# Kernel tuning notes

Measured on AMD Instinct MI355X. Metric: run time of the kernel, lower is better.

Reference implementation:

```python
import jax, jax.numpy as jnp
import numpy as np

N_QUBITS = 8   # out_channels = number of wires
KERNEL = 4     # kernel_size
N_LAYERS = 4
STRIDE = 1
PAD = 1


def _rx(t):
    c = jnp.cos(t * 0.5).astype(jnp.complex64)
    s = jnp.sin(t * 0.5).astype(jnp.complex64)
    return jnp.stack([jnp.stack([c, -1j * s]), jnp.stack([-1j * s, c])])


def _ry(t):
    c = jnp.cos(t * 0.5).astype(jnp.complex64)
    s = jnp.sin(t * 0.5).astype(jnp.complex64)
    return jnp.stack([jnp.stack([c, -s]), jnp.stack([s, c])])


def _rz(t):
    e = jnp.exp(-0.5j * t.astype(jnp.complex64))
    z = jnp.zeros((), jnp.complex64)
    return jnp.stack([jnp.stack([e, z]), jnp.stack([z, jnp.conj(e)])])


def _ap1(state, U, w):
    # apply 2x2 gate U on qubit axis w of state shaped (2,)*N_QUBITS
    s = jnp.moveaxis(state, w, -1)
    s = s @ U.T
    return jnp.moveaxis(s, -1, w)


def _cnot(state, c, t):
    s0 = jax.lax.index_in_dim(state, 0, axis=c, keepdims=True)
    s1 = jax.lax.index_in_dim(state, 1, axis=c, keepdims=True)
    return jnp.concatenate([s0, jnp.flip(s1, axis=t)], axis=c)


def _ansatz(state, wl):  # wl: (N_QUBITS, 3) angles for layer i (custom_layers)
    for j in range(N_QUBITS):
        c, t = (j, j + 1) if j < N_QUBITS - 1 else (0, j)
        state = _ap1(state, _rx(wl[j, 0]), j)
        state = _cnot(state, c, t)
        state = _ap1(state, _ry(wl[j, 1]), j)
        state = _cnot(state, c, t)
        state = _ap1(state, _rz(wl[j, 2]), j)
    return state


def _circuit(inputs, weights):
    # inputs: (KERNEL,) patch; weights: (N_LAYERS+1, N_QUBITS, 3)
    state = jnp.zeros((2,) * N_QUBITS, jnp.complex64).at[(0,) * N_QUBITS].set(1.0)
    state = _ansatz(state, weights[0])
    for i in range(1, N_LAYERS + 1):
        w = 0
        for _ in range(N_QUBITS // KERNEL):  # 'parallel': re-upload data each layer
            for k in range(KERNEL):
                state = _ap1(state, _ry(inputs[k]), w + k)
            w += KERNEL
        state = _ansatz(state, weights[i])
    probs = state.real ** 2 + state.imag ** 2
    sign = jnp.array([1.0, -1.0], jnp.float32)
    z = [jnp.sum(probs, axis=tuple(a for a in range(N_QUBITS) if a != j)) @ sign
         for j in range(N_QUBITS)]
    return jnp.stack(z)  # (N_QUBITS,) <PauliZ_j>


def _forward(vector, weights):
    bs, ch, l = vector.shape
    if ch > 1:
        vector = vector.mean(axis=-2).reshape(bs, 1, l)
    v = jnp.pad(vector, ((0, 0), (0, 0), (PAD, PAD)))
    l_out = (l + 2 * PAD - KERNEL) // STRIDE + 1
    idx = jnp.arange(l_out)[:, None] * STRIDE + jnp.arange(KERNEL)  # (l_out, K)
    patches = v[:, 0, :][:, idx].reshape(bs * l_out, KERNEL)
    q = jax.vmap(_circuit, in_axes=(0, None))(patches, weights)  # (bs*l_out, N_QUBITS)
    out = q.reshape(bs, l_out, N_QUBITS).transpose(0, 2, 1)  # (bs, C, l_out)
    out = jax.nn.relu(out)
    return jnp.max(out, axis=-1, keepdims=True)  # (bs, C, 1)


def setup_inputs() -> dict:
    key = jax.random.key(0)
    k1, k2 = jax.random.split(key)
    vector = jax.random.normal(k1, (8, 1, 512), jnp.float32)
    # flax nn.initializers.normal() default stddev = 0.01
    weights = jax.random.normal(k2, (N_LAYERS + 1, N_QUBITS, 3), jnp.float32) * 0.01
    return {"vector": vector, "weights": weights}


def reference(vector, weights):
    return _forward(vector, weights)
```

## Files before the change

kernel.cpp:

```cpp
#include <hip/hip_runtime.h>

#define NQ 8
#define KK 4
#define LIN 512
#define LOUT 511
#define BATCH 8
#define NCIRC (BATCH * LOUT)

__device__ float g_tab[240];
__device__ float g_st0[512];

template<int M> __device__ __forceinline__ float lx(float v) {
    if constexpr (M == 1)
        return __builtin_bit_cast(float, __builtin_amdgcn_update_dpp(
            0, __builtin_bit_cast(int, v), 0xB1, 0xF, 0xF, true));
    else if constexpr (M == 2)
        return __builtin_bit_cast(float, __builtin_amdgcn_update_dpp(
            0, __builtin_bit_cast(int, v), 0x4E, 0xF, 0xF, true));
    else if constexpr (M == 3)
        return __builtin_bit_cast(float, __builtin_amdgcn_update_dpp(
            0, __builtin_bit_cast(int, v), 0x1B, 0xF, 0xF, true));
    else if constexpr (M < 32)
        return __builtin_bit_cast(float, __builtin_amdgcn_ds_swizzle(
            __builtin_bit_cast(int, v), (M << 10) | 0x1F));
    else
        return __shfl_xor(v, M, 64);
}

template<int BP>
__device__ __forceinline__ void g_rx4(float (&sr)[4], float (&si)[4], float c, float s, int lane) {
    if constexpr (BP >= 2) {
        constexpr int M = 1 << (BP - 2);
        #pragma unroll
        for (int r = 0; r < 4; ++r) {
            float orr = lx<M>(sr[r]), oii = lx<M>(si[r]);
            float nr = c * sr[r] + s * oii;
            float ni = c * si[r] - s * orr;
            sr[r] = nr; si[r] = ni;
        }
    } else if constexpr (BP == 1) {
        #pragma unroll
        for (int p = 0; p < 2; ++p) {
            const int a = p, b = p + 2;
            float ar = sr[a], ai = si[a], br = sr[b], bi = si[b];
            sr[a] = c*ar + s*bi;  si[a] = c*ai - s*br;
            sr[b] = c*br + s*ai;  si[b] = c*bi - s*ar;
        }
    } else {
        #pragma unroll
        for (int p = 0; p < 2; ++p) {
            const int a = 2*p, b = 2*p + 1;
            float ar = sr[a], ai = si[a], br = sr[b], bi = si[b];
            sr[a] = c*ar + s*bi;  si[a] = c*ai - s*br;
            sr[b] = c*br + s*ai;  si[b] = c*bi - s*ar;
        }
    }
}

template<int BP>
__device__ __forceinline__ void g_rz4(float (&sr)[4], float (&si)[4], float c, float s, int lane) {
    if constexpr (BP >= 2) {
        const float t = ((lane >> (BP - 2)) & 1) ? -s : s;
        #pragma unroll
        for (int r = 0; r < 4; ++r) {
            float nr = c * sr[r] + t * si[r];
            float ni = c * si[r] - t * sr[r];
            sr[r] = nr; si[r] = ni;
        }
    } else if constexpr (BP == 1) {
        #pragma unroll
        for (int r = 0; r < 4; ++r) {
            const float t = (r < 2) ? s : -s;
            float nr = c * sr[r] + t * si[r];
            float ni = c * si[r] - t * sr[r];
            sr[r] = nr; si[r] = ni;
        }
    } else {
        #pragma unroll
        for (int r = 0; r < 4; ++r) {
            const float t = ((r & 1) == 0) ? s : -s;
            float nr = c * sr[r] + t * si[r];
            float ni = c * si[r] - t * sr[r];
            sr[r] = nr; si[r] = ni;
        }
    }
}

template<int BPC, int BPT>
__device__ __forceinline__ void g_fry4(float (&sr)[4], float (&si)[4], float c, float s, int lane) {
    if constexpr (BPT >= 2) {
        constexpr int M = (1 << (BPC - 2)) | (1 << (BPT - 2));
        const float sg = ((lane >> (BPC - 2)) & 1) ? s : -s;
        #pragma unroll
        for (int r = 0; r < 4; ++r) {
            float orr = lx<M>(sr[r]), oii = lx<M>(si[r]);
            sr[r] = c * sr[r] + sg * orr;
            si[r] = c * si[r] + sg * oii;
        }
    } else if constexpr (BPT == 1) {
        constexpr int M = 1 << (BPC - 2);
        const float sg = ((lane >> (BPC - 2)) & 1) ? s : -s;
        float pr[4], pi[4];
        #pragma unroll
        for (int r = 0; r < 4; ++r) { pr[r] = lx<M>(sr[r ^ 2]); pi[r] = lx<M>(si[r ^ 2]); }
        #pragma unroll
        for (int r = 0; r < 4; ++r) { sr[r] = c*sr[r] + sg*pr[r]; si[r] = c*si[r] + sg*pi[r]; }
    } else if constexpr (BPC == 1) {
        float t0r = sr[0], t0i = si[0], t1r = sr[1], t1i = si[1];
        sr[0] = c*sr[0] - s*sr[3];  si[0] = c*si[0] - s*si[3];
        sr[1] = c*sr[1] - s*sr[2];  si[1] = c*si[1] - s*si[2];
        sr[2] = c*sr[2] + s*t1r;    si[2] = c*si[2] + s*t1i;
        sr[3] = c*sr[3] + s*t0r;    si[3] = c*si[3] + s*t0i;
    } else {
        constexpr int M = 1 << (BPC - 2);
        const float sg = ((lane >> (BPC - 2)) & 1) ? s : -s;
        float pr[4], pi[4];
        #pragma unroll
        for (int r = 0; r < 4; ++r) { pr[r] = lx<M>(sr[r ^ 1]); pi[r] = lx<M>(si[r ^ 1]); }
        #pragma unroll
        for (int r = 0; r < 4; ++r) { sr[r] = c*sr[r] + sg*pr[r]; si[r] = c*si[r] + sg*pi[r]; }
    }
}

template<int J>
__device__ __forceinline__ void astep4(float (&sr)[4], float (&si)[4],
                                       const float* __restrict__ t48, int lane) {
    constexpr int CQ = (J < 7) ? J : 0;
    constexpr int TQ = (J < 7) ? (J + 1) : 7;
    constexpr int BP = 7 - J, BPC = 7 - CQ, BPT = 7 - TQ;
    g_rx4<BP>(sr, si, t48[J*6 + 0], t48[J*6 + 1], lane);
    g_fry4<BPC, BPT>(sr, si, t48[J*6 + 2], t48[J*6 + 3], lane);
    g_rz4<BP>(sr, si, t48[J*6 + 4], t48[J*6 + 5], lane);
}

template<int LB>
__device__ __forceinline__ void rx_lane(float (&sr)[16], float (&si)[16], float c, float s) {
    constexpr int M = 1 << LB;
    #pragma unroll
    for (int r = 0; r < 16; ++r) {
        float orr = lx<M>(sr[r]), oii = lx<M>(si[r]);
        float nr = c * sr[r] + s * oii;
        float ni = c * si[r] - s * orr;
        sr[r] = nr; si[r] = ni;
    }
}

template<int LB>
__device__ __forceinline__ void ry_lane(float (&sr)[16], float (&si)[16], float c, float s, int pos) {
    constexpr int M = 1 << LB;
    const float sg = ((pos >> LB) & 1) ? s : -s;
    #pragma unroll
    for (int r = 0; r < 16; ++r) {
        float orr = lx<M>(sr[r]), oii = lx<M>(si[r]);
        sr[r] = c * sr[r] + sg * orr;
        si[r] = c * si[r] + sg * oii;
    }
}

template<int LB>
__device__ __forceinline__ void rz_lane(float (&sr)[16], float (&si)[16], float c, float s, int pos) {
    const float t = ((pos >> LB) & 1) ? -s : s;
    #pragma unroll
    for (int r = 0; r < 16; ++r) {
        float nr = c * sr[r] + t * si[r];
        float ni = c * si[r] - t * sr[r];
        sr[r] = nr; si[r] = ni;
    }
}

template<int RB>
__device__ __forceinline__ void rx_reg(float (&sr)[16], float (&si)[16], float c, float s) {
    constexpr int m = 1 << RB;
    #pragma unroll
    for (int r = 0; r < 16; ++r) {
        if ((r & m) == 0) {
            const int a = r, b = r | m;
            float ar = sr[a], ai = si[a], br = sr[b], bi = si[b];
            sr[a] = c*ar + s*bi;  si[a] = c*ai - s*br;
            sr[b] = c*br + s*ai;  si[b] = c*bi - s*ar;
        }
    }
}

template<int RB>
__device__ __forceinline__ void ry_reg(float (&sr)[16], float (&si)[16], float c, float s) {
    constexpr int m = 1 << RB;
    #pragma unroll
    for (int r = 0; r < 16; ++r) {
        if ((r & m) == 0) {
            const int a = r, b = r | m;
            float ar = sr[a], ai = si[a], br = sr[b], bi = si[b];
            sr[a] = c*ar - s*br;  si[a] = c*ai - s*bi;
            sr[b] = s*ar + c*br;  si[b] = s*ai + c*bi;
        }
    }
}

template<int RB>
__device__ __forceinline__ void rz_reg(float (&sr)[16], float (&si)[16], float c, float s) {
    #pragma unroll
    for (int r = 0; r < 16; ++r) {
        const float t = ((r >> RB) & 1) ? -s : s;
        float nr = c * sr[r] + t * si[r];
        float ni = c * si[r] - t * sr[r];
        sr[r] = nr; si[r] = ni;
    }
}

template<int LBc, int LBt>
__device__ __forceinline__ void fry_ll(float (&sr)[16], float (&si)[16], float c, float s, int pos) {
    constexpr int M = (1 << LBc) | (1 << LBt);
    const float sg = ((pos >> LBc) & 1) ? s : -s;
    #pragma unroll
    for (int r = 0; r < 16; ++r) {
        float orr = lx<M>(sr[r]), oii = lx<M>(si[r]);
        sr[r] = c * sr[r] + sg * orr;
        si[r] = c * si[r] + sg * oii;
    }
}

template<int LBc, int RBt>
__device__ __forceinline__ void fry_lr(float (&sr)[16], float (&si)[16], float c, float s, int pos) {
    constexpr int M = 1 << LBc;
    constexpr int mt = 1 << RBt;
    const float sg = ((pos >> LBc) & 1) ? s : -s;
    float pr[16], pi[16];
    #pragma unroll
    for (int r = 0; r < 16; ++r) { pr[r] = lx<M>(sr[r ^ mt]); pi[r] = lx<M>(si[r ^ mt]); }
    #pragma unroll
    for (int r = 0; r < 16; ++r) { sr[r] = c*sr[r] + sg*pr[r]; si[r] = c*si[r] + sg*pi[r]; }
}

template<int RBc, int RBt>
__device__ __forceinline__ void fry_rr(float (&sr)[16], float (&si)[16], float c, float s) {
    constexpr int mm = (1 << RBc) | (1 << RBt);
    float nr[16], ni[16];
    #pragma unroll
    for (int r = 0; r < 16; ++r) {
        const float sg = ((r >> RBc) & 1) ? s : -s;
        nr[r] = c*sr[r] + sg*sr[r ^ mm];
        ni[r] = c*si[r] + sg*si[r ^ mm];
    }
    #pragma unroll
    for (int r = 0; r < 16; ++r) { sr[r] = nr[r]; si[r] = ni[r]; }
}

__device__ __forceinline__ void ansatz16(float (&sr)[16], float (&si)[16],
                                         const float* __restrict__ t, int pos) {
    rx_lane<3>(sr, si, t[0], t[1]);   fry_ll<3,2>(sr, si, t[2], t[3], pos);   rz_lane<3>(sr, si, t[4], t[5], pos);
    rx_lane<2>(sr, si, t[6], t[7]);   fry_ll<2,1>(sr, si, t[8], t[9], pos);   rz_lane<2>(sr, si, t[10], t[11], pos);
    rx_lane<1>(sr, si, t[12], t[13]); fry_ll<1,0>(sr, si, t[14], t[15], pos); rz_lane<1>(sr, si, t[16], t[17], pos);
    rx_lane<0>(sr, si, t[18], t[19]); fry_lr<0,3>(sr, si, t[20], t[21], pos); rz_lane<0>(sr, si, t[22], t[23], pos);
    rx_reg<3>(sr, si, t[24], t[25]);  fry_rr<3,2>(sr, si, t[26], t[27]);      rz_reg<3>(sr, si, t[28], t[29]);
    rx_reg<2>(sr, si, t[30], t[31]);  fry_rr<2,1>(sr, si, t[32], t[33]);      rz_reg<2>(sr, si, t[34], t[35]);
    rx_reg<1>(sr, si, t[36], t[37]);  fry_rr<1,0>(sr, si, t[38], t[39]);      rz_reg<1>(sr, si, t[40], t[41]);
    rx_reg<0>(sr, si, t[42], t[43]);  fry_lr<3,0>(sr, si, t[44], t[45], pos); rz_reg<0>(sr, si, t[46], t[47]);
}

__device__ __forceinline__ void reup16(float (&sr)[16], float (&si)[16],
                                       const float (&xc)[4], const float (&xs)[4], int pos) {
    ry_lane<3>(sr, si, xc[0], xs[0], pos);  ry_reg<3>(sr, si, xc[0], xs[0]);
    ry_lane<2>(sr, si, xc[1], xs[1], pos);  ry_reg<2>(sr, si, xc[1], xs[1]);
    ry_lane<1>(sr, si, xc[2], xs[2], pos);  ry_reg<1>(sr, si, xc[2], xs[2]);
    ry_lane<0>(sr, si, xc[3], xs[3], pos);  ry_reg<0>(sr, si, xc[3], xs[3]);
}

template<int ST>
__device__ __forceinline__ void bstage16(float (&z)[8], int pos) {
    constexpr int M = 1 << ST;
    #pragma unroll
    for (int q = 0; q < 8; ++q) {
        float o = lx<M>(z[q]);
        if (q < 4 && (3 - q) == ST)
            z[q] = ((pos >> ST) & 1) ? (o - z[q]) : (z[q] - o);
        else
            z[q] += o;
    }
}

__global__ __launch_bounds__(256) void prep_kernel(const float* __restrict__ wts,
                                                   float* __restrict__ out) {
    __shared__ float tt[240];
    const int t = threadIdx.x;
    if (t < 120) {
        float a = 0.5f * wts[t];
        float cv = __cosf(a), sv = __sinf(a);
        g_tab[2*t] = cv;  g_tab[2*t + 1] = sv;
        tt[2*t] = cv;     tt[2*t + 1] = sv;
    }
    if (t >= 192 && t < 192 + BATCH * NQ) out[t - 192] = 0.0f;
    __syncthreads();
    if (t < 64) {
        const int lane = t;
        float sr[4] = {0.f, 0.f, 0.f, 0.f};
        float si[4] = {0.f, 0.f, 0.f, 0.f};
        if (lane == 0) sr[0] = 1.0f;
        astep4<0>(sr, si, tt, lane); astep4<1>(sr, si, tt, lane);
        astep4<2>(sr, si, tt, lane); astep4<3>(sr, si, tt, lane);
        astep4<4>(sr, si, tt, lane); astep4<5>(sr, si, tt, lane);
        astep4<6>(sr, si, tt, lane); astep4<7>(sr, si, tt, lane);
        #pragma unroll
        for (int r = 0; r < 4; ++r) {
            g_st0[(lane*4 + r)*2]     = sr[r];
            g_st0[(lane*4 + r)*2 + 1] = si[r];
        }
    }
}

__global__ __launch_bounds__(256, 1) void quanv_kernel(const float* __restrict__ vec,
                                                       float* __restrict__ out) {
    const int tid = threadIdx.x;
    const int pos = tid & 15;
    int circ = blockIdx.x * 16 + (tid >> 4);
    if (circ > NCIRC - 1) circ = NCIRC - 1;
    const int b = circ / LOUT;
    const int op = circ - b * LOUT;

    float xc[4], xs[4];
    #pragma unroll
    for (int k = 0; k < KK; ++k) {
        int idx = op - 1 + k;
        int ic = idx < 0 ? 0 : (idx > LIN - 1 ? LIN - 1 : idx);
        float xv = vec[b * LIN + ic];
        xv = (idx == ic) ? xv : 0.0f;
        float a = 0.5f * xv;
        xs[k] = __sinf(a); xc[k] = __cosf(a);
    }

    float sr[16], si[16];
    {
        const float4* st4 = (const float4*)g_st0;
        #pragma unroll
        for (int h = 0; h < 8; ++h) {
            float4 v4 = st4[pos * 8 + h];
            sr[2*h]   = v4.x; si[2*h]   = v4.y;
            sr[2*h+1] = v4.z; si[2*h+1] = v4.w;
        }
    }

    #pragma unroll 1
    for (int L = 1; L <= 4; ++L) {
        reup16(sr, si, xc, xs, pos);
        ansatz16(sr, si, g_tab + L * 48, pos);
    }

    float p[16];
    #pragma unroll
    for (int r = 0; r < 16; ++r) p[r] = sr[r]*sr[r] + si[r]*si[r];
    float pl = 0.f, z4 = 0.f, z5 = 0.f, z6 = 0.f, z7 = 0.f;
    #pragma unroll
    for (int r = 0; r < 16; ++r) {
        pl += p[r];
        z4 += ((r >> 3) & 1) ? -p[r] : p[r];
        z5 += ((r >> 2) & 1) ? -p[r] : p[r];
        z6 += ((r >> 1) & 1) ? -p[r] : p[r];
        z7 += ( r       & 1) ? -p[r] : p[r];
    }
    float z[8];
    z[0] = pl; z[1] = pl; z[2] = pl; z[3] = pl;
    z[4] = z4; z[5] = z5; z[6] = z6; z[7] = z7;

    bstage16<0>(z, pos); bstage16<1>(z, pos); bstage16<2>(z, pos); bstage16<3>(z, pos);

    __shared__ float zsh[16][NQ];
    __shared__ int bsh[16];
    const int g = tid >> 4;
    if (pos == 0) {
        bsh[g] = b;
        #pragma unroll
        for (int q = 0; q < NQ; ++q) zsh[g][q] = fmaxf(z[q], 0.0f);
    }
    __syncthreads();
    if (tid < 128) {
        const int gg = tid >> 3, q = tid & 7;
        const bool leader = (gg == 0) || (bsh[gg] != bsh[gg - 1]);
        if (leader) {
            float m = zsh[gg][q];
            for (int g2 = gg + 1; g2 < 16 && bsh[g2] == bsh[gg]; ++g2)
                m = fmaxf(m, zsh[g2][q]);
            atomicMax((unsigned int*)(out + bsh[gg] * NQ + q), __float_as_uint(m));
        }
    }
}

extern "C" void kernel_launch(void* const* d_in, const int* in_sizes, int n_in,
                              void* d_out, int out_size, void* d_ws, size_t ws_size,
                              hipStream_t stream) {
    const float* vec = (const float*)d_in[0];
    const float* wts = (const float*)d_in[1];
    float* out = (float*)d_out;

    hipLaunchKernelGGL(prep_kernel, dim3(1), dim3(256), 0, stream, wts, out);
    const int blocks = (NCIRC + 15) / 16;
    hipLaunchKernelGGL(quanv_kernel, dim3(blocks), dim3(256), 0, stream, vec, out);
}
```

Before: 79.95 us.

## Split each circuit's statevector across 32 lanes with 8 amplitudes per thread

Each simulated circuit now uses 32 threads holding 8 complex amplitudes each instead of 16 threads holding 16, so one more qubit is mapped onto lanes and handled with cross-lane DPP/swizzle exchanges. This halves the per-thread register state and drops the launch-bounds occupancy limit of 1, which should allow more waves per CU. The last layer's RZ gates are skipped because they only change phases and do not affect the Z expectations, and the final CNOT-RY-CNOT is rewritten as a controlled-sign RY. The trade-off is more cross-lane shuffles per gate, a different reduction tree, and twice as many blocks.

```diff
diff --git a/kernel.cpp b/kernel.cpp
--- a/kernel.cpp
+++ b/kernel.cpp
@@ -20,6 +20,9 @@
     else if constexpr (M == 3)
         return __builtin_bit_cast(float, __builtin_amdgcn_update_dpp(
             0, __builtin_bit_cast(int, v), 0x1B, 0xF, 0xF, true));
+    else if constexpr (M == 8)
+        return __builtin_bit_cast(float, __builtin_amdgcn_update_dpp(
+            0, __builtin_bit_cast(int, v), 0x128, 0xF, 0xF, true));
     else if constexpr (M < 32)
         return __builtin_bit_cast(float, __builtin_amdgcn_ds_swizzle(
             __builtin_bit_cast(int, v), (M << 10) | 0x1F));
@@ -122,22 +125,35 @@
     }
 }
 
+__device__ __forceinline__ void g_cry4_q7(float (&sr)[4], float (&si)[4], float c, float s, int lane) {
+    const float se = ((lane >> 5) & 1) ? -s : s;
+    #pragma unroll
+    for (int p = 0; p < 2; ++p) {
+        const int a = 2*p, b = 2*p + 1;
+        float ar = sr[a], ai = si[a], br = sr[b], bi = si[b];
+        sr[a] = c*ar - se*br;  si[a] = c*ai - se*bi;
+        sr[b] = se*ar + c*br;  si[b] = se*ai + c*bi;
+    }
+}
+
 template<int J>
 __device__ __forceinline__ void astep4(float (&sr)[4], float (&si)[4],
                                        const float* __restrict__ t48, int lane) {
-    constexpr int CQ = (J < 7) ? J : 0;
-    constexpr int TQ = (J < 7) ? (J + 1) : 7;
-    constexpr int BP = 7 - J, BPC = 7 - CQ, BPT = 7 - TQ;
+    constexpr int BP = 7 - J;
     g_rx4<BP>(sr, si, t48[J*6 + 0], t48[J*6 + 1], lane);
-    g_fry4<BPC, BPT>(sr, si, t48[J*6 + 2], t48[J*6 + 3], lane);
+    if constexpr (J < 7) {
+        g_fry4<7 - J, 6 - J>(sr, si, t48[J*6 + 2], t48[J*6 + 3], lane);
+    } else {
+        g_cry4_q7(sr, si, t48[J*6 + 2], t48[J*6 + 3], lane);
+    }
     g_rz4<BP>(sr, si, t48[J*6 + 4], t48[J*6 + 5], lane);
 }
 
 template<int LB>
-__device__ __forceinline__ void rx_lane(float (&sr)[16], float (&si)[16], float c, float s) {
+__device__ __forceinline__ void rx_lane(float (&sr)[8], float (&si)[8], float c, float s) {
     constexpr int M = 1 << LB;
     #pragma unroll
-    for (int r = 0; r < 16; ++r) {
+    for (int r = 0; r < 8; ++r) {
         float orr = lx<M>(sr[r]), oii = lx<M>(si[r]);
         float nr = c * sr[r] + s * oii;
         float ni = c * si[r] - s * orr;
@@ -146,11 +162,11 @@
 }
 
 template<int LB>
-__device__ __forceinline__ void ry_lane(float (&sr)[16], float (&si)[16], float c, float s, int pos) {
+__device__ __forceinline__ void ry_lane(float (&sr)[8], float (&si)[8], float c, float s, int lane) {
     constexpr int M = 1 << LB;
-    const float sg = ((pos >> LB) & 1) ? s : -s;
-    #pragma unroll
-    for (int r = 0; r < 16; ++r) {
+    const float sg = ((lane >> LB) & 1) ? s : -s;
+    #pragma unroll
+    for (int r = 0; r < 8; ++r) {
         float orr = lx<M>(sr[r]), oii = lx<M>(si[r]);
         sr[r] = c * sr[r] + sg * orr;
         si[r] = c * si[r] + sg * oii;
@@ -158,10 +174,10 @@
 }
 
 template<int LB>
-__device__ __forceinline__ void rz_lane(float (&sr)[16], float (&si)[16], float c, float s, int pos) {
-    const float t = ((pos >> LB) & 1) ? -s : s;
-    #pragma unroll
-    for (int r = 0; r < 16; ++r) {
+__device__ __forceinline__ void rz_lane(float (&sr)[8], float (&si)[8], float c, float s, int lane) {
+    const float t = ((lane >> LB) & 1) ? -s : s;
+    #pragma unroll
+    for (int r = 0; r < 8; ++r) {
         float nr = c * sr[r] + t * si[r];
         float ni = c * si[r] - t * sr[r];
         sr[r] = nr; si[r] = ni;
@@ -169,10 +185,10 @@
 }
 
 template<int RB>
-__device__ __forceinline__ void rx_reg(float (&sr)[16], float (&si)[16], float c, float s) {
+__device__ __forceinline__ void rx_reg(float (&sr)[8], float (&si)[8], float c, float s) {
     constexpr int m = 1 << RB;
     #pragma unroll
-    for (int r = 0; r < 16; ++r) {
+    for (int r = 0; r < 8; ++r) {
         if ((r & m) == 0) {
             const int a = r, b = r | m;
             float ar = sr[a], ai = si[a], br = sr[b], bi = si[b];
@@ -183,10 +199,10 @@
 }
 
 template<int RB>
-__device__ __forceinline__ void ry_reg(float (&sr)[16], float (&si)[16], float c, float s) {
+__device__ __forceinline__ void ry_reg(float (&sr)[8], float (&si)[8], float c, float s) {
     constexpr int m = 1 << RB;
     #pragma unroll
-    for (int r = 0; r < 16; ++r) {
+    for (int r = 0; r < 8; ++r) {
         if ((r & m) == 0) {
             const int a = r, b = r | m;
             float ar = sr[a], ai = si[a], br = sr[b], bi = si[b];
@@ -197,9 +213,9 @@
 }
 
 template<int RB>
-__device__ __forceinline__ void rz_reg(float (&sr)[16], float (&si)[16], float c, float s) {
-    #pragma unroll
-    for (int r = 0; r < 16; ++r) {
+__device__ __forceinline__ void rz_reg(float (&sr)[8], float (&si)[8], float c, float s) {
+    #pragma unroll
+    for (int r = 0; r < 8; ++r) {
         const float t = ((r >> RB) & 1) ? -s : s;
         float nr = c * sr[r] + t * si[r];
         float ni = c * si[r] - t * sr[r];
@@ -208,11 +224,11 @@
 }
 
 template<int LBc, int LBt>
-__device__ __forceinline__ void fry_ll(float (&sr)[16], float (&si)[16], float c, float s, int pos) {
+__device__ __forceinline__ void fry_ll(float (&sr)[8], float (&si)[8], float c, float s, int lane) {
     constexpr int M = (1 << LBc) | (1 << LBt);
-    const float sg = ((pos >> LBc) & 1) ? s : -s;
-    #pragma unroll
-    for (int r = 0; r < 16; ++r) {
+    const float sg = ((lane >> LBc) & 1) ? s : -s;
+    #pragma unroll
+    for (int r = 0; r < 8; ++r) {
         float orr = lx<M>(sr[r]), oii = lx<M>(si[r]);
         sr[r] = c * sr[r] + sg * orr;
         si[r] = c * si[r] + sg * oii;
@@ -220,59 +236,87 @@
 }
 
 template<int LBc, int RBt>
-__device__ __forceinline__ void fry_lr(float (&sr)[16], float (&si)[16], float c, float s, int pos) {
+__device__ __forceinline__ void fry_lr(float (&sr)[8], float (&si)[8], float c, float s, int lane) {
     constexpr int M = 1 << LBc;
     constexpr int mt = 1 << RBt;
-    const float sg = ((pos >> LBc) & 1) ? s : -s;
-    float pr[16], pi[16];
-    #pragma unroll
-    for (int r = 0; r < 16; ++r) { pr[r] = lx<M>(sr[r ^ mt]); pi[r] = lx<M>(si[r ^ mt]); }
-    #pragma unroll
-    for (int r = 0; r < 16; ++r) { sr[r] = c*sr[r] + sg*pr[r]; si[r] = c*si[r] + sg*pi[r]; }
+    const float sg = ((lane >> LBc) & 1) ? s : -s;
+    float pr[8], pi[8];
+    #pragma unroll
+    for (int r = 0; r < 8; ++r) { pr[r] = lx<M>(sr[r ^ mt]); pi[r] = lx<M>(si[r ^ mt]); }
+    #pragma unroll
+    for (int r = 0; r < 8; ++r) { sr[r] = c*sr[r] + sg*pr[r]; si[r] = c*si[r] + sg*pi[r]; }
 }
 
 template<int RBc, int RBt>
-__device__ __forceinline__ void fry_rr(float (&sr)[16], float (&si)[16], float c, float s) {
+__device__ __forceinline__ void fry_rr(float (&sr)[8], float (&si)[8], float c, float s) {
     constexpr int mm = (1 << RBc) | (1 << RBt);
-    float nr[16], ni[16];
-    #pragma unroll
-    for (int r = 0; r < 16; ++r) {
+    float nr[8], ni[8];
+    #pragma unroll
+    for (int r = 0; r < 8; ++r) {
         const float sg = ((r >> RBc) & 1) ? s : -s;
         nr[r] = c*sr[r] + sg*sr[r ^ mm];
         ni[r] = c*si[r] + sg*si[r ^ mm];
     }
     #pragma unroll
-    for (int r = 0; r < 16; ++r) { sr[r] = nr[r]; si[r] = ni[r]; }
-}
-
-__device__ __forceinline__ void ansatz16(float (&sr)[16], float (&si)[16],
-                                         const float* __restrict__ t, int pos) {
-    rx_lane<3>(sr, si, t[0], t[1]);   fry_ll<3,2>(sr, si, t[2], t[3], pos);   rz_lane<3>(sr, si, t[4], t[5], pos);
-    rx_lane<2>(sr, si, t[6], t[7]);   fry_ll<2,1>(sr, si, t[8], t[9], pos);   rz_lane<2>(sr, si, t[10], t[11], pos);
-    rx_lane<1>(sr, si, t[12], t[13]); fry_ll<1,0>(sr, si, t[14], t[15], pos); rz_lane<1>(sr, si, t[16], t[17], pos);
-    rx_lane<0>(sr, si, t[18], t[19]); fry_lr<0,3>(sr, si, t[20], t[21], pos); rz_lane<0>(sr, si, t[22], t[23], pos);
-    rx_reg<3>(sr, si, t[24], t[25]);  fry_rr<3,2>(sr, si, t[26], t[27]);      rz_reg<3>(sr, si, t[28], t[29]);
-    rx_reg<2>(sr, si, t[30], t[31]);  fry_rr<2,1>(sr, si, t[32], t[33]);      rz_reg<2>(sr, si, t[34], t[35]);
-    rx_reg<1>(sr, si, t[36], t[37]);  fry_rr<1,0>(sr, si, t[38], t[39]);      rz_reg<1>(sr, si, t[40], t[41]);
-    rx_reg<0>(sr, si, t[42], t[43]);  fry_lr<3,0>(sr, si, t[44], t[45], pos); rz_reg<0>(sr, si, t[46], t[47]);
-}
-
-__device__ __forceinline__ void reup16(float (&sr)[16], float (&si)[16],
-                                       const float (&xc)[4], const float (&xs)[4], int pos) {
-    ry_lane<3>(sr, si, xc[0], xs[0], pos);  ry_reg<3>(sr, si, xc[0], xs[0]);
-    ry_lane<2>(sr, si, xc[1], xs[1], pos);  ry_reg<2>(sr, si, xc[1], xs[1]);
-    ry_lane<1>(sr, si, xc[2], xs[2], pos);  ry_reg<1>(sr, si, xc[2], xs[2]);
-    ry_lane<0>(sr, si, xc[3], xs[3], pos);  ry_reg<0>(sr, si, xc[3], xs[3]);
+    for (int r = 0; r < 8; ++r) { sr[r] = nr[r]; si[r] = ni[r]; }
+}
+
+__device__ __forceinline__ void cry_q7(float (&sr)[8], float (&si)[8], float c, float s, int lane) {
+    const float se = ((lane >> 4) & 1) ? -s : s;
+    #pragma unroll
+    for (int p = 0; p < 4; ++p) {
+        const int a = 2*p, b = 2*p + 1;
+        float ar = sr[a], ai = si[a], br = sr[b], bi = si[b];
+        sr[a] = c*ar - se*br;  si[a] = c*ai - se*bi;
+        sr[b] = se*ar + c*br;  si[b] = se*ai + c*bi;
+    }
+}
+
+template<bool LAST>
+__device__ __forceinline__ void ansatz8(float (&sr)[8], float (&si)[8],
+                                        const float* __restrict__ t, int lane) {
+    rx_lane<4>(sr, si, t[0], t[1]);
+    fry_ll<4,3>(sr, si, t[2], t[3], lane);
+    if (!LAST) rz_lane<4>(sr, si, t[4], t[5], lane);
+    rx_lane<3>(sr, si, t[6], t[7]);
+    fry_ll<3,2>(sr, si, t[8], t[9], lane);
+    if (!LAST) rz_lane<3>(sr, si, t[10], t[11], lane);
+    rx_lane<2>(sr, si, t[12], t[13]);
+    fry_ll<2,1>(sr, si, t[14], t[15], lane);
+    if (!LAST) rz_lane<2>(sr, si, t[16], t[17], lane);
+    rx_lane<1>(sr, si, t[18], t[19]);
+    fry_ll<1,0>(sr, si, t[20], t[21], lane);
+    if (!LAST) rz_lane<1>(sr, si, t[22], t[23], lane);
+    rx_lane<0>(sr, si, t[24], t[25]);
+    fry_lr<0,2>(sr, si, t[26], t[27], lane);
+    if (!LAST) rz_lane<0>(sr, si, t[28], t[29], lane);
+    rx_reg<2>(sr, si, t[30], t[31]);
+    fry_rr<2,1>(sr, si, t[32], t[33]);
+    if (!LAST) rz_reg<2>(sr, si, t[34], t[35]);
+    rx_reg<1>(sr, si, t[36], t[37]);
+    fry_rr<1,0>(sr, si, t[38], t[39]);
+    if (!LAST) rz_reg<1>(sr, si, t[40], t[41]);
+    rx_reg<0>(sr, si, t[42], t[43]);
+    cry_q7(sr, si, t[44], t[45], lane);
+    if (!LAST) rz_reg<0>(sr, si, t[46], t[47]);
+}
+
+__device__ __forceinline__ void reup8(float (&sr)[8], float (&si)[8],
+                                      const float (&xc)[4], const float (&xs)[4], int lane) {
+    ry_lane<4>(sr, si, xc[0], xs[0], lane);  ry_lane<0>(sr, si, xc[0], xs[0], lane);
+    ry_lane<3>(sr, si, xc[1], xs[1], lane);  ry_reg<2>(sr, si, xc[1], xs[1]);
+    ry_lane<2>(sr, si, xc[2], xs[2], lane);  ry_reg<1>(sr, si, xc[2], xs[2]);
+    ry_lane<1>(sr, si, xc[3], xs[3], lane);  ry_reg<0>(sr, si, xc[3], xs[3]);
 }
 
 template<int ST>
-__device__ __forceinline__ void bstage16(float (&z)[8], int pos) {
+__device__ __forceinline__ void bstage8(float (&z)[8], int lane) {
     constexpr int M = 1 << ST;
     #pragma unroll
     for (int q = 0; q < 8; ++q) {
         float o = lx<M>(z[q]);
-        if (q < 4 && (3 - q) == ST)
-            z[q] = ((pos >> ST) & 1) ? (o - z[q]) : (z[q] - o);
+        if (q < 5 && (4 - q) == ST)
+            z[q] = ((lane >> ST) & 1) ? (o - z[q]) : (z[q] - o);
         else
             z[q] += o;
     }
@@ -307,12 +351,12 @@
     }
 }
 
-__global__ __launch_bounds__(256, 1) void quanv_kernel(const float* __restrict__ vec,
-                                                       float* __restrict__ out) {
+__global__ __launch_bounds__(256) void quanv_kernel(const float* __restrict__ vec,
+                                                    float* __restrict__ out) {
     const int tid = threadIdx.x;
-    const int pos = tid & 15;
-    int circ = blockIdx.x * 16 + (tid >> 4);
-    if (circ > NCIRC - 1) circ = NCIRC - 1;
+    const int lane = tid & 63;
+    const int pos = tid & 31;
+    const int circ = blockIdx.x * 8 + (tid >> 5);
     const int b = circ / LOUT;
     const int op = circ - b * LOUT;
 
@@ -327,56 +371,58 @@
         xs[k] = __sinf(a); xc[k] = __cosf(a);
     }
 
-    float sr[16], si[16];
+    float sr[8], si[8];
     {
         const float4* st4 = (const float4*)g_st0;
         #pragma unroll
-        for (int h = 0; h < 8; ++h) {
-            float4 v4 = st4[pos * 8 + h];
+        for (int h = 0; h < 4; ++h) {
+            float4 v4 = st4[pos * 4 + h];
             sr[2*h]   = v4.x; si[2*h]   = v4.y;
             sr[2*h+1] = v4.z; si[2*h+1] = v4.w;
         }
     }
 
     #pragma unroll 1
-    for (int L = 1; L <= 4; ++L) {
-        reup16(sr, si, xc, xs, pos);
-        ansatz16(sr, si, g_tab + L * 48, pos);
-    }
-
-    float p[16];
-    #pragma unroll
-    for (int r = 0; r < 16; ++r) p[r] = sr[r]*sr[r] + si[r]*si[r];
-    float pl = 0.f, z4 = 0.f, z5 = 0.f, z6 = 0.f, z7 = 0.f;
-    #pragma unroll
-    for (int r = 0; r < 16; ++r) {
+    for (int L = 1; L <= 3; ++L) {
+        reup8(sr, si, xc, xs, lane);
+        ansatz8<false>(sr, si, g_tab + L * 48, lane);
+    }
+    reup8(sr, si, xc, xs, lane);
+    ansatz8<true>(sr, si, g_tab + 4 * 48, lane);
+
+    float p[8];
+    #pragma unroll
+    for (int r = 0; r < 8; ++r) p[r] = sr[r]*sr[r] + si[r]*si[r];
+    float pl = 0.f, z5 = 0.f, z6 = 0.f, z7 = 0.f;
+    #pragma unroll
+    for (int r = 0; r < 8; ++r) {
         pl += p[r];
-        z4 += ((r >> 3) & 1) ? -p[r] : p[r];
         z5 += ((r >> 2) & 1) ? -p[r] : p[r];
         z6 += ((r >> 1) & 1) ? -p[r] : p[r];
         z7 += ( r       & 1) ? -p[r] : p[r];
     }
     float z[8];
-    z[0] = pl; z[1] = pl; z[2] = pl; z[3] = pl;
-    z[4] = z4; z[5] = z5; z[6] = z6; z[7] = z7;
-
-    bstage16<0>(z, pos); bstage16<1>(z, pos); bstage16<2>(z, pos); bstage16<3>(z, pos);
-
-    __shared__ float zsh[16][NQ];
-    __shared__ int bsh[16];
-    const int g = tid >> 4;
+    z[0] = pl; z[1] = pl; z[2] = pl; z[3] = pl; z[4] = pl;
+    z[5] = z5; z[6] = z6; z[7] = z7;
+
+    bstage8<0>(z, lane); bstage8<1>(z, lane); bstage8<2>(z, lane);
+    bstage8<3>(z, lane); bstage8<4>(z, lane);
+
+    __shared__ float zsh[8][NQ];
+    __shared__ int bsh[8];
+    const int g = tid >> 5;
     if (pos == 0) {
         bsh[g] = b;
         #pragma unroll
         for (int q = 0; q < NQ; ++q) zsh[g][q] = fmaxf(z[q], 0.0f);
     }
     __syncthreads();
-    if (tid < 128) {
+    if (tid < 64) {
         const int gg = tid >> 3, q = tid & 7;
         const bool leader = (gg == 0) || (bsh[gg] != bsh[gg - 1]);
         if (leader) {
             float m = zsh[gg][q];
-            for (int g2 = gg + 1; g2 < 16 && bsh[g2] == bsh[gg]; ++g2)
+            for (int g2 = gg + 1; g2 < 8 && bsh[g2] == bsh[gg]; ++g2)
                 m = fmaxf(m, zsh[g2][q]);
             atomicMax((unsigned int*)(out + bsh[gg] * NQ + q), __float_as_uint(m));
         }
@@ -391,6 +437,6 @@
     float* out = (float*)d_out;
 
     hipLaunchKernelGGL(prep_kernel, dim3(1), dim3(256), 0, stream, wts, out);
-    const int blocks = (NCIRC + 15) / 16;
+    const int blocks = NCIRC / 8;
     hipLaunchKernelGGL(quanv_kernel, dim3(blocks), dim3(256), 0, stream, vec, out);
 }
```

Result: faster. 75.45 us (-5.6%).
